# Performance work log

Measured on AMD Instinct MI355X. Metric: run time of the kernel, lower is better.

## Reference

```python
import jax, jax.numpy as jnp
import numpy as np

COMMA_ID = 1010  # ',' in bert-base-uncased vocab
N_HEADS = 8
BN_EPS = 1e-5


def setup_inputs() -> dict:
    key = jax.random.key(0)
    ks = jax.random.split(key, 12)
    B, S, D = 64, 512, 768
    sc = 0.02
    text_hs = jax.random.normal(ks[0], (B, S, D), jnp.float32)
    cols_hs = jax.random.normal(ks[1], (B, S, D), jnp.float32)
    # column input ids: random non-comma tokens, commas planted every 16 positions -> 32 commas/row, 33 segments
    col_ids = jax.random.randint(ks[2], (B, S), 2000, 30000, dtype=jnp.int32)
    col_ids = col_ids.at[:, ::16].set(COMMA_ID)
    Wq = jax.random.normal(ks[3], (D, D), jnp.float32) * sc
    Wk = jax.random.normal(ks[4], (D, D), jnp.float32) * sc
    Wv = jax.random.normal(ks[5], (D, D), jnp.float32) * sc
    Wo = jax.random.normal(ks[6], (D, D), jnp.float32) * sc
    bq = jnp.zeros((D,), jnp.float32)
    bk = jnp.zeros((D,), jnp.float32)
    bv = jnp.zeros((D,), jnp.float32)
    bo = jnp.zeros((D,), jnp.float32)
    gamma = jnp.ones((S,), jnp.float32)
    beta = jnp.zeros((S,), jnp.float32)
    w_out = jax.random.normal(ks[7], (D, 1), jnp.float32) * sc
    b_out = jnp.zeros((1,), jnp.float32)
    return {"text_hs": text_hs, "cols_hs": cols_hs, "col_ids": col_ids, "n_segments": 33,
            "Wq": Wq, "bq": bq, "Wk": Wk, "bk": bk, "Wv": Wv, "bv": bv, "Wo": Wo, "bo": bo,
            "gamma": gamma, "beta": beta, "w_out": w_out, "b_out": b_out}


def reference(text_hs, cols_hs, col_ids, n_segments,
              Wq, bq, Wk, bk, Wv, bv, Wo, bo, gamma, beta, w_out, b_out):
    B, S, D = text_hs.shape
    hd = D // N_HEADS
    # cross attention: query = columns, key/value = text (torch MultiheadAttention, batch_first)
    q = (cols_hs @ Wq.T + bq).reshape(B, S, N_HEADS, hd)
    k = (text_hs @ Wk.T + bk).reshape(B, S, N_HEADS, hd)
    v = (text_hs @ Wv.T + bv).reshape(B, S, N_HEADS, hd)
    scores = jnp.einsum('bqhd,bkhd->bhqk', q, k) / jnp.sqrt(jnp.asarray(hd, q.dtype))
    attn = jax.nn.softmax(scores, axis=-1)
    o = jnp.einsum('bhqk,bkhd->bqhd', attn, v).reshape(B, S, D)
    attn_out = o @ Wo.T + bo  # [B,S,D]
    # BatchNorm1d(S) in training mode: per-seq-position channel stats over (batch, D)
    mean = attn_out.mean(axis=(0, 2), keepdims=True)
    var = jnp.mean((attn_out - mean) ** 2, axis=(0, 2), keepdims=True)
    bn = (attn_out - mean) / jnp.sqrt(var + BN_EPS) * gamma[None, :, None] + beta[None, :, None]
    # residual add + scalar head -> per-token score [B,S]
    ret = ((cols_hs + bn) @ w_out + b_out)[..., 0]
    # compose_outputs: segment-sum over comma-delimited spans, comma tokens excluded
    is_comma = col_ids == COMMA_ID
    seg = jnp.cumsum(is_comma.astype(jnp.int32), axis=1)  # commas before each non-comma token
    vals = jnp.where(is_comma, jnp.zeros((), ret.dtype), ret)
    flat_seg = (jnp.arange(B, dtype=jnp.int32)[:, None] * n_segments + seg).reshape(-1)
    out = jax.ops.segment_sum(vals.reshape(-1), flat_seg, num_segments=B * n_segments)
    return out.reshape(B, n_segments)
```

## Files before the change

kernel.cpp:

```cpp
#include <hip/hip_runtime.h>
#include <hip/hip_bf16.h>
#include <math.h>

typedef __attribute__((ext_vector_type(8))) short bf16x8;
typedef __attribute__((ext_vector_type(4))) float f32x4;

#define COMMA_ID 1010
#define S 512
#define D 768
#define NH 8
#define HD 96

__device__ __forceinline__ ushort f2bf(float f) {
  union { float f; unsigned u; } v; v.f = f;
  unsigned u = v.u;
  return (ushort)((u + 0x7fffu + ((u >> 16) & 1u)) >> 16);
}
__device__ __forceinline__ float bf2f(ushort h) {
  union { unsigned u; float f; } v; v.u = ((unsigned)h) << 16; return v.f;
}

__device__ __forceinline__ void async16(void* lds, const void* g) {
  __builtin_amdgcn_global_load_lds(
      (const __attribute__((address_space(1))) unsigned int*)g,
      (__attribute__((address_space(3))) unsigned int*)lds, 16, 0, 0);
}

__device__ __forceinline__ f32x4 mfma16(bf16x8 a, bf16x8 b, f32x4 c) {
  return __builtin_amdgcn_mfma_f32_16x16x32_bf16(a, b, c, 0, 0, 0);
}

__global__ __launch_bounds__(256) void cvt2_kernel(const float* __restrict__ a, ushort* __restrict__ oa,
                                                   const float* __restrict__ b, ushort* __restrict__ ob_,
                                                   int n8each) {
  int i = blockIdx.x * 256 + threadIdx.x;
  const float* in; ushort* out; int j;
  if (i < n8each) { in = a; out = oa; j = i; }
  else { in = b; out = ob_; j = i - n8each; if (j >= n8each) return; }
  const float4* p = ((const float4*)in) + (size_t)j * 2;
  float4 x = p[0], y = p[1];
  bf16x8 o;
  o[0] = (short)f2bf(x.x); o[1] = (short)f2bf(x.y); o[2] = (short)f2bf(x.z); o[3] = (short)f2bf(x.w);
  o[4] = (short)f2bf(y.x); o[5] = (short)f2bf(y.y); o[6] = (short)f2bf(y.z); o[7] = (short)f2bf(y.w);
  ((bf16x8*)out)[j] = o;
}

__global__ __launch_bounds__(256) void cvtW_kernel(
    const float* __restrict__ w0, const float* __restrict__ w1,
    const float* __restrict__ w2, const float* __restrict__ w3,
    ushort* __restrict__ o0, ushort* __restrict__ o1,
    ushort* __restrict__ o2, ushort* __restrict__ o3,
    int n8, float sc0) {
  int i = blockIdx.x * 256 + threadIdx.x;
  int sel = i / n8, j = i - sel * n8;
  if (sel >= 4) return;
  const float* in = sel == 0 ? w0 : sel == 1 ? w1 : sel == 2 ? w2 : w3;
  ushort* out = sel == 0 ? o0 : sel == 1 ? o1 : sel == 2 ? o2 : o3;
  float sc = sel == 0 ? sc0 : 1.0f;
  const float4* p = ((const float4*)in) + (size_t)j * 2;
  float4 x = p[0], y = p[1];
  bf16x8 o;
  o[0] = (short)f2bf(x.x * sc); o[1] = (short)f2bf(x.y * sc); o[2] = (short)f2bf(x.z * sc); o[3] = (short)f2bf(x.w * sc);
  o[4] = (short)f2bf(y.x * sc); o[5] = (short)f2bf(y.y * sc); o[6] = (short)f2bf(y.z * sc); o[7] = (short)f2bf(y.w * sc);
  ((bf16x8*)out)[j] = o;
}

#define BM 128
#define BN 128
#define BK 64
#define KDIM 768
#define NDIM 768

template<int MODE>
__global__ __launch_bounds__(256, 3) void gemm_bf16(
    const ushort* __restrict__ A, const ushort* __restrict__ W,
    const float* __restrict__ bias0, const float* __restrict__ bias1,
    float bscale, ushort* __restrict__ C0, ushort* __restrict__ C1,
    const float* __restrict__ wv, float* __restrict__ sum_s,
    float* __restrict__ sq_s, float* __restrict__ c2,
    int M, int NTILES)
{
  int nwg = gridDim.x, cpx = nwg >> 3;
  int l = (blockIdx.x & 7) * cpx + (blockIdx.x >> 3);
  int mt = l / NTILES, nt = l % NTILES;
  int m0 = mt * BM, n0 = nt * BN;
  int sel = n0 >= NDIM;
  int cbase = n0 - (sel ? NDIM : 0);
  const float* bi = sel ? bias1 : bias0;
  ushort* Co = sel ? C1 : C0;
  int tid = threadIdx.x;
  int w = tid >> 6, lane = tid & 63;
  int wr = w >> 1, wc = w & 1;
  int lr = lane & 15, ks = lane >> 4;
  __shared__ __align__(16) ushort As[BM * BK];
  __shared__ __align__(16) ushort Bs[BN * BK];
  f32x4 acc[4][4] = {};
  const ushort* Arow = A + (size_t)m0 * KDIM;
  const ushort* Wrow = W + (size_t)n0 * KDIM;
  int srow = tid >> 3, sch = tid & 7;

  auto STAGE = [&](int k0) {
#pragma unroll
    for (int i = 0; i < 4; ++i) {
      int row = i * 32 + srow;
      int scc = sch ^ (row & 7);
      async16(&As[(row * 8 + sch) * 8], Arow + (size_t)row * KDIM + k0 + scc * 8);
      async16(&Bs[(row * 8 + sch) * 8], Wrow + (size_t)row * KDIM + k0 + scc * 8);
    }
  };
  auto COMPUTE = [&]() {
    bf16x8 a[4][2], b[4][2];
#pragma unroll
    for (int m = 0; m < 4; m++) {
      int row = wr * 64 + m * 16 + lr;
#pragma unroll
      for (int kk = 0; kk < 2; kk++) {
        int cc = kk * 4 + ks;
        a[m][kk] = *(const bf16x8*)&As[(row * 8 + (cc ^ (row & 7))) * 8];
      }
    }
#pragma unroll
    for (int n = 0; n < 4; n++) {
      int row = wc * 64 + n * 16 + lr;
#pragma unroll
      for (int kk = 0; kk < 2; kk++) {
        int cc = kk * 4 + ks;
        b[n][kk] = *(const bf16x8*)&Bs[(row * 8 + (cc ^ (row & 7))) * 8];
      }
    }
#pragma unroll
    for (int m = 0; m < 4; m++)
#pragma unroll
      for (int n = 0; n < 4; n++) {
        acc[m][n] = mfma16(a[m][0], b[n][0], acc[m][n]);
        acc[m][n] = mfma16(a[m][1], b[n][1], acc[m][n]);
      }
  };

  for (int k0 = 0; k0 < KDIM; k0 += BK) {
    STAGE(k0);
    __syncthreads();
    COMPUTE();
    __syncthreads();
  }

  float bnv[4];
#pragma unroll
  for (int n = 0; n < 4; n++) bnv[n] = bi[cbase + wc * 64 + n * 16 + lr] * bscale;

  if (MODE == 0) {
#pragma unroll
    for (int m = 0; m < 4; m++) {
      int grow = m0 + wr * 64 + m * 16 + ks * 4;
#pragma unroll
      for (int r = 0; r < 4; r++) {
        ushort* cp = Co + (size_t)(grow + r) * NDIM + cbase + wc * 64 + lr;
#pragma unroll
        for (int n = 0; n < 4; n++) cp[n * 16] = f2bf(acc[m][n][r] + bnv[n]);
      }
    }
  } else {
    float wn[4];
#pragma unroll
    for (int n = 0; n < 4; n++) wn[n] = wv[cbase + wc * 64 + n * 16 + lr];
#pragma unroll
    for (int m = 0; m < 4; m++) {
#pragma unroll
      for (int r = 0; r < 4; r++) {
        float ps = 0.f, pq = 0.f, pw = 0.f;
#pragma unroll
        for (int n = 0; n < 4; n++) {
          float v = acc[m][n][r] + bnv[n];
          ps += v; pq += v * v; pw += v * wn[n];
        }
#pragma unroll
        for (int mk = 1; mk < 16; mk <<= 1) {
          ps += __shfl_xor(ps, mk);
          pq += __shfl_xor(pq, mk);
          pw += __shfl_xor(pw, mk);
        }
        if (lr == 0) {
          int grow = m0 + wr * 64 + m * 16 + ks * 4 + r;
          atomicAdd(&sum_s[grow & (S - 1)], ps);
          atomicAdd(&sq_s[grow & (S - 1)], pq);
          atomicAdd(&c2[grow], pw);
        }
      }
    }
  }
}

__global__ __launch_bounds__(256) void transpose_v(const ushort* __restrict__ vb,
                                                   ushort* __restrict__ vt) {
  int blk = blockIdx.x;
  int dt = blk % 3; int st = (blk / 3) % (S / 32); int h = (blk / (3 * (S / 32))) % NH;
  int b = blk / (3 * (S / 32) * NH);
  __shared__ ushort t[32][33];
  int i = threadIdx.x >> 5, j = threadIdx.x & 31;
  int s0 = st * 32, d0 = dt * 32;
#pragma unroll
  for (int k = 0; k < 4; k++) {
    int s = s0 + i + k * 8;
    t[i + k * 8][j] = vb[((size_t)(b * S + s)) * D + h * HD + d0 + j];
  }
  __syncthreads();
#pragma unroll
  for (int k = 0; k < 4; k++) {
    int d = d0 + i + k * 8;
    vt[((size_t)((b * NH + h) * HD + d)) * S + s0 + j] = t[j][i + k * 8];
  }
}

__global__ __launch_bounds__(256, 3) void attn_kernel(const ushort* __restrict__ qb,
                                                      const ushort* __restrict__ kb,
                                                      const ushort* __restrict__ vt,
                                                      ushort* __restrict__ ob) {
  int wgid = blockIdx.x;
  int xcd = wgid & 7, t1 = wgid >> 3;
  int qt = t1 & 3, phi = t1 >> 2;
  int p = phi * 8 + xcd;
  int b = p >> 3, h = p & 7;
  int tid = threadIdx.x;
  int w = tid >> 6, lane = tid & 63;
  int lr = lane & 15, ks = lane >> 4;
  int q0 = qt * 128 + w * 32;

  __shared__ __align__(16) ushort Ks[6144];
  __shared__ __align__(16) ushort Vs[2][6144];
  __shared__ __align__(16) ushort Pb[4][1152];
  ushort* Pw = &Pb[w][0];

  const size_t bS = (size_t)b * S;
  const ushort* qptr = qb + (bS + q0 + lr) * D + h * HD;
  bf16x8 aq[2][3];
#pragma unroll
  for (int m = 0; m < 2; m++)
#pragma unroll
    for (int x = 0; x < 3; x++)
      aq[m][x] = *(const bf16x8*)(qptr + (size_t)m * 16 * D + x * 32 + ks * 8);

  float l_part[2][4] = {};
  f32x4 oacc[2][6] = {};

  const ushort* kbase = kb + bS * D + h * HD;
  const ushort* vbase = vt + (size_t)((b * NH + h) * HD) * S;

  auto STAGE_K = [&](int kv0) {
#pragma unroll
    for (int i = 0; i < 3; i++) {
      int c = w + 4 * i;
      async16(&Ks[(c * 64 + lane) * 8], kbase + (size_t)(kv0 + lane) * D + c * 8);
    }
  };
  auto STAGE_V = [&](int buf, int kv0) {
#pragma unroll
    for (int i = 0; i < 3; i++) {
      int u = (w + 4 * i) * 64 + lane;
      int cc = u / 96, d = u - cc * 96;
      async16(&Vs[buf][(size_t)u * 8], vbase + (size_t)d * S + kv0 + cc * 8);
    }
  };

  STAGE_K(0);
  STAGE_V(0, 0);
  __syncthreads();

  for (int it = 0; it < 8; ++it) {
    int cur = it & 1;
    f32x4 st[2][4];
#pragma unroll
    for (int t = 0; t < 4; t++) {
      bf16x8 bk[3];
#pragma unroll
      for (int x = 0; x < 3; x++)
        bk[x] = *(const bf16x8*)&Ks[((x * 4 + ks) * 64 + t * 16 + lr) * 8];
#pragma unroll
      for (int m = 0; m < 2; m++) {
        f32x4 s = {};
        s = mfma16(aq[m][0], bk[0], s);
        s = mfma16(aq[m][1], bk[1], s);
        s = mfma16(aq[m][2], bk[2], s);
        st[m][t] = s;
      }
    }
    __syncthreads();
    if (it < 7) { STAGE_K((it + 1) * 64); STAGE_V(cur ^ 1, (it + 1) * 64); }
    bf16x8 pa[2][2];
#pragma unroll
    for (int m = 0; m < 2; m++) {
#pragma unroll
      for (int t = 0; t < 4; t++)
#pragma unroll
        for (int r = 0; r < 4; r++) {
          float e = exp2f(st[m][t][r]);
          l_part[m][r] += e;
          Pw[(ks * 4 + r) * 72 + t * 16 + lr] = f2bf(e);
        }
#pragma unroll
      for (int kk = 0; kk < 2; kk++)
        pa[m][kk] = *(const bf16x8*)&Pw[lr * 72 + kk * 32 + ks * 8];
    }
    const ushort* Vb = &Vs[cur][0];
#pragma unroll
    for (int kk = 0; kk < 2; kk++)
#pragma unroll
      for (int n = 0; n < 6; n++) {
        bf16x8 bv = *(const bf16x8*)&Vb[((kk * 4 + ks) * 96 + n * 16 + lr) * 8];
        oacc[0][n] = mfma16(pa[0][kk], bv, oacc[0][n]);
        oacc[1][n] = mfma16(pa[1][kk], bv, oacc[1][n]);
      }
    __syncthreads();
  }

  float inv[2][4];
#pragma unroll
  for (int m = 0; m < 2; m++)
#pragma unroll
    for (int r = 0; r < 4; r++) {
      float s = l_part[m][r];
#pragma unroll
      for (int mk = 1; mk < 16; mk <<= 1) s += __shfl_xor(s, mk);
      inv[m][r] = 1.0f / s;
    }
  ushort* optr = ob + (bS + q0) * D + h * HD;
#pragma unroll
  for (int m = 0; m < 2; m++)
#pragma unroll
    for (int n = 0; n < 6; n++)
#pragma unroll
      for (int r = 0; r < 4; r++)
        optr[(size_t)(m * 16 + ks * 4 + r) * D + n * 16 + lr] = f2bf(oacc[m][n][r] * inv[m][r]);
}

__global__ __launch_bounds__(256) void c1_dot(const ushort* __restrict__ colsb,
                                              const float* __restrict__ wv,
                                              float* __restrict__ c1) {
  int row = blockIdx.x * 4 + (threadIdx.x >> 6);
  int lane = threadIdx.x & 63;
  const ushort* rp = colsb + (size_t)row * D;
  float s = 0.f;
  bf16x8 a = *(const bf16x8*)(rp + lane * 8);
#pragma unroll
  for (int j = 0; j < 8; j++) s += bf2f((ushort)a[j]) * wv[lane * 8 + j];
  ushort4 b4 = *(const ushort4*)(rp + 512 + lane * 4);
  s += bf2f(b4.x) * wv[512 + lane * 4 + 0];
  s += bf2f(b4.y) * wv[512 + lane * 4 + 1];
  s += bf2f(b4.z) * wv[512 + lane * 4 + 2];
  s += bf2f(b4.w) * wv[512 + lane * 4 + 3];
#pragma unroll
  for (int mk = 1; mk < 64; mk <<= 1) s += __shfl_xor(s, mk);
  if (lane == 0) c1[row] = s;
}

__global__ __launch_bounds__(512) void finalize_kernel(
    const float* __restrict__ sum_s, const float* __restrict__ sq_s,
    const float* __restrict__ c1, const float* __restrict__ c2,
    const float* __restrict__ gamma, const float* __restrict__ beta,
    const float* __restrict__ wv, const float* __restrict__ b_out,
    const int* __restrict__ ids, float* __restrict__ out, int nseg, float invBD)
{
  int b = blockIdx.x, s = threadIdx.x;
  int wid = s >> 6, lane = s & 63;
  __shared__ float wpart[8];
  __shared__ int wtot[8];
  __shared__ float seg_acc[64];
  float wval = wv[s] + (s < (D - S) ? wv[S + s] : 0.f);
  float t = wval;
#pragma unroll
  for (int mk = 1; mk < 64; mk <<= 1) t += __shfl_xor(t, mk);
  if (lane == 0) wpart[wid] = t;
  int row = b * S + s;
  bool comma = (ids[row] == COMMA_ID);
  unsigned long long mask = __ballot(comma);
  if (lane == 0) wtot[wid] = __popcll(mask);
  if (s < 64) seg_acc[s] = 0.f;
  __syncthreads();
  float Sw = 0.f;
#pragma unroll
  for (int i = 0; i < 8; i++) Sw += wpart[i];
  float mean = sum_s[s] * invBD;
  float var = sq_s[s] * invBD - mean * mean;
  float alpha = gamma[s] * rsqrtf(var + 1e-5f);
  float shift = beta[s] - mean * alpha;
  float ret = c1[row] + b_out[0] + alpha * c2[row] + shift * Sw;
  int base = 0;
  for (int i = 0; i < wid; i++) base += wtot[i];
  int seg = base + __popcll(mask & ((1ull << lane) - 1ull)) + (comma ? 1 : 0);
  if (!comma && seg < nseg) atomicAdd(&seg_acc[seg], ret);
  __syncthreads();
  if (s < nseg) out[b * nseg + s] = seg_acc[s];
}

extern "C" void kernel_launch(void* const* d_in, const int* in_sizes, int n_in,
                              void* d_out, int out_size, void* d_ws, size_t ws_size,
                              hipStream_t stream) {
  const float* text = (const float*)d_in[0];
  const float* cols = (const float*)d_in[1];
  const int* ids = (const int*)d_in[2];
  const float* Wq = (const float*)d_in[4];
  const float* bq = (const float*)d_in[5];
  const float* Wk = (const float*)d_in[6];
  const float* bk = (const float*)d_in[7];
  const float* Wv = (const float*)d_in[8];
  const float* bv = (const float*)d_in[9];
  const float* Wo = (const float*)d_in[10];
  const float* bo = (const float*)d_in[11];
  const float* gamma = (const float*)d_in[12];
  const float* beta = (const float*)d_in[13];
  const float* wv = (const float*)d_in[14];
  const float* b_out = (const float*)d_in[15];

  const int B = in_sizes[0] / (S * D);
  const int M = B * S;
  const int nseg = out_size / B;
  const size_t NE = (size_t)B * S * D;
  const size_t big = NE * 2;
  const float qscale = 0.10206207262f * 1.44269504089f;

  char* ws = (char*)d_ws;
  size_t off = 0;
  auto alloc = [&](size_t bytes) { void* p = ws + off; off = (off + bytes + 255) & ~(size_t)255; return p; };
  ushort* ws0 = (ushort*)alloc(big);
  ushort* ws1 = (ushort*)alloc(big);
  ushort* qb  = (ushort*)alloc(big);
  ushort* kb  = (ushort*)alloc(big);
  ushort* Wq_b = (ushort*)alloc((size_t)D * D * 2);
  ushort* Wk_b = (ushort*)alloc((size_t)D * D * 2);
  ushort* Wv_b = (ushort*)alloc((size_t)D * D * 2);
  ushort* Wo_b = (ushort*)alloc((size_t)D * D * 2);
  float* sum_s = (float*)alloc(S * 4);
  float* sq_s  = (float*)alloc(S * 4);
  float* c1    = (float*)alloc((size_t)M * 4);
  float* c2    = (float*)alloc((size_t)M * 4);

  ushort* text_b = ws0; ushort* cols_b = ws1;
  ushort* vb = ws1;
  ushort* vt = ws0;
  ushort* ob = ws1;

  int n8 = (int)(NE / 8);
  cvt2_kernel<<<(2 * n8 + 255) / 256, 256, 0, stream>>>(text, text_b, cols, cols_b, n8);
  int w8 = D * D / 8;
  cvtW_kernel<<<(4 * w8 + 255) / 256, 256, 0, stream>>>(Wq, Wk, Wv, Wo, Wq_b, Wk_b, Wv_b, Wo_b, w8, qscale);

  hipMemsetAsync(sum_s, 0, S * 4, stream);
  hipMemsetAsync(sq_s, 0, S * 4, stream);
  hipMemsetAsync(c2, 0, (size_t)M * 4, stream);

  c1_dot<<<M / 4, 256, 0, stream>>>(cols_b, wv, c1);

  int g6 = (M / BM) * 6;
  int g12 = (M / BM) * 12;
  gemm_bf16<0><<<g6, 256, 0, stream>>>(cols_b, Wq_b, bq, bq, qscale, qb, qb,
                                       nullptr, nullptr, nullptr, nullptr, M, 6);
  gemm_bf16<0><<<g12, 256, 0, stream>>>(text_b, Wk_b, bk, bv, 1.0f, kb, vb,
                                        nullptr, nullptr, nullptr, nullptr, M, 12);

  transpose_v<<<B * NH * (S / 32) * 3, 256, 0, stream>>>(vb, vt);

  attn_kernel<<<B * NH * 4, 256, 0, stream>>>(qb, kb, vt, ob);

  gemm_bf16<1><<<g6, 256, 0, stream>>>(ob, Wo_b, bo, bo, 1.0f, nullptr, nullptr,
                                       wv, sum_s, sq_s, c2, M, 6);

  finalize_kernel<<<B, 512, 0, stream>>>(sum_s, sq_s, c1, c2, gamma, beta, wv, b_out, ids,
                                         (float*)d_out, nseg, 1.0f / (float)(B * D));
}
```

Measured before the change: 421.6 us.

## Merge Q and K/V projection GEMMs into one launch and raise occupancy bound

The Q projection and the fused K/V projection now run as a single grid: blocks below a split index handle Q from the column states, and the rest handle K/V from the text states. When the workspace allows, V gets its own buffer so it no longer aliases the column-state input that the Q blocks still read. The launch bound rises from 3 to 4 waves per SIMD, which could force fewer registers and cause spills. The aim is to remove one launch and the tail idle between the two GEMMs.

```diff
diff --git a/kernel.cpp b/kernel.cpp
--- a/kernel.cpp
+++ b/kernel.cpp
@@ -72,22 +72,30 @@
 #define NDIM 768
 
 template<int MODE>
-__global__ __launch_bounds__(256, 3) void gemm_bf16(
-    const ushort* __restrict__ A, const ushort* __restrict__ W,
+__global__ __launch_bounds__(256, 4) void gemm_bf16(
+    const ushort* __restrict__ A0, const ushort* __restrict__ A1,
+    const ushort* __restrict__ W0, const ushort* __restrict__ W1,
     const float* __restrict__ bias0, const float* __restrict__ bias1,
-    float bscale, ushort* __restrict__ C0, ushort* __restrict__ C1,
+    const float* __restrict__ bias2, float bscale0,
+    ushort* __restrict__ C0, ushort* __restrict__ C1, ushort* __restrict__ C2,
     const float* __restrict__ wv, float* __restrict__ sum_s,
     float* __restrict__ sq_s, float* __restrict__ c2,
-    int M, int NTILES)
+    int qblocks, int NT0, int NT1)
 {
   int nwg = gridDim.x, cpx = nwg >> 3;
   int l = (blockIdx.x & 7) * cpx + (blockIdx.x >> 3);
-  int mt = l / NTILES, nt = l % NTILES;
+  int seg1 = (l >= qblocks);
+  int ls = seg1 ? l - qblocks : l;
+  int NTILES = seg1 ? NT1 : NT0;
+  const ushort* A = seg1 ? A1 : A0;
+  const ushort* W = seg1 ? W1 : W0;
+  float bscale = seg1 ? 1.0f : bscale0;
+  int mt = ls / NTILES, nt = ls % NTILES;
   int m0 = mt * BM, n0 = nt * BN;
-  int sel = n0 >= NDIM;
+  int sel = (n0 >= NDIM);
   int cbase = n0 - (sel ? NDIM : 0);
-  const float* bi = sel ? bias1 : bias0;
-  ushort* Co = sel ? C1 : C0;
+  const float* bi = seg1 ? (sel ? bias2 : bias1) : bias0;
+  ushort* Co = seg1 ? (sel ? C2 : C1) : C0;
   int tid = threadIdx.x;
   int w = tid >> 6, lane = tid & 63;
   int wr = w >> 1, wc = w & 1;
@@ -432,9 +440,11 @@
   float* sq_s  = (float*)alloc(S * 4);
   float* c1    = (float*)alloc((size_t)M * 4);
   float* c2    = (float*)alloc((size_t)M * 4);
+  bool merged = (off + big) <= ws_size;
+  ushort* vbig = merged ? (ushort*)alloc(big) : nullptr;
 
   ushort* text_b = ws0; ushort* cols_b = ws1;
-  ushort* vb = ws1;
+  ushort* vb = merged ? vbig : ws1;
   ushort* vt = ws0;
   ushort* ob = ws1;
 
@@ -449,19 +459,37 @@
 
   c1_dot<<<M / 4, 256, 0, stream>>>(cols_b, wv, c1);
 
-  int g6 = (M / BM) * 6;
-  int g12 = (M / BM) * 12;
-  gemm_bf16<0><<<g6, 256, 0, stream>>>(cols_b, Wq_b, bq, bq, qscale, qb, qb,
-                                       nullptr, nullptr, nullptr, nullptr, M, 6);
-  gemm_bf16<0><<<g12, 256, 0, stream>>>(text_b, Wk_b, bk, bv, 1.0f, kb, vb,
-                                        nullptr, nullptr, nullptr, nullptr, M, 12);
+  int qblocks = (M / BM) * 6;
+  if (merged) {
+    int gall = qblocks + (M / BM) * 12;
+    gemm_bf16<0><<<gall, 256, 0, stream>>>(cols_b, text_b, Wq_b, Wk_b,
+                                           bq, bk, bv, qscale,
+                                           qb, kb, vb,
+                                           nullptr, nullptr, nullptr, nullptr,
+                                           qblocks, 6, 12);
+  } else {
+    gemm_bf16<0><<<qblocks, 256, 0, stream>>>(cols_b, cols_b, Wq_b, Wq_b,
+                                              bq, bq, bq, qscale,
+                                              qb, qb, qb,
+                                              nullptr, nullptr, nullptr, nullptr,
+                                              qblocks, 6, 6);
+    int g12 = (M / BM) * 12;
+    gemm_bf16<0><<<g12, 256, 0, stream>>>(text_b, text_b, Wk_b, Wk_b,
+                                          bk, bk, bv, 1.0f,
+                                          kb, kb, vb,
+                                          nullptr, nullptr, nullptr, nullptr,
+                                          0, 12, 12);
+  }
 
   transpose_v<<<B * NH * (S / 32) * 3, 256, 0, stream>>>(vb, vt);
 
   attn_kernel<<<B * NH * 4, 256, 0, stream>>>(qb, kb, vt, ob);
 
-  gemm_bf16<1><<<g6, 256, 0, stream>>>(ob, Wo_b, bo, bo, 1.0f, nullptr, nullptr,
-                                       wv, sum_s, sq_s, c2, M, 6);
+  gemm_bf16<1><<<qblocks, 256, 0, stream>>>(ob, ob, Wo_b, Wo_b,
+                                            bo, bo, bo, 1.0f,
+                                            nullptr, nullptr, nullptr,
+                                            wv, sum_s, sq_s, c2,
+                                            qblocks, 6, 6);
 
   finalize_kernel<<<B, 512, 0, stream>>>(sum_s, sq_s, c1, c2, gamma, beta, wv, b_out, ids,
                                          (float*)d_out, nseg, 1.0f / (float)(B * D));
```

Measured after the change: 446.4 us. 1.06x slower.
